# Kernel tuning notes

Measured on AMD Instinct MI355X. Metric: run time of the kernel, lower is better.

## Reference

```python
import jax, jax.numpy as jnp
import numpy as np

EMB = 128   # embedding_dim
ND = 128    # node_dim
B = 64      # graphs in batch
NN = 500    # n_nodes per graph
N = B * NN  # total nodes = 32000
E = 256000  # edges per edge set
M = 20      # history length in input_


def _lin_params(key, out_dim, in_dim, bias=True):
    k1, k2 = jax.random.split(key)
    s = 1.0 / np.sqrt(in_dim)
    w = jax.random.uniform(k1, (out_dim, in_dim), jnp.float32, -s, s)
    if bias:
        b = jax.random.uniform(k2, (out_dim,), jnp.float32, -s, s)
        return w, b
    return w


def setup_inputs() -> dict:
    key = jax.random.key(0)
    ks = jax.random.split(key, 40)
    inp = {}
    inp["state_"] = jax.random.normal(ks[0], (B, ND), jnp.float32)
    inp["input_"] = jax.random.normal(ks[1], (B, M, EMB), jnp.float32)
    inp["x"] = jax.random.normal(ks[2], (N, EMB), jnp.float32)
    inp["e_n"] = jax.random.randint(ks[3], (2, E), 0, N)
    inp["e_r0"] = jax.random.randint(ks[4], (2, E), 0, N)
    inp["e_r1"] = jax.random.randint(ks[5], (2, E), 0, N)
    inp["n_nodes"] = NN
    # GRU-like params
    inp["win"] = _lin_params(ks[6], ND, EMB, bias=False)
    inp["wz"], inp["bz"] = _lin_params(ks[7], ND, 2 * ND)
    inp["wr"], inp["br"] = _lin_params(ks[8], ND, 2 * ND)
    inp["wh"], inp["bh"] = _lin_params(ks[9], ND, 2 * ND)
    # GAT params: lin (out,in)+bias, attn (out, 2*out)+bias
    inp["g0_lw"], inp["g0_lb"] = _lin_params(ks[10], ND, EMB)
    inp["g0_aw"], inp["g0_ab"] = _lin_params(ks[11], ND, 2 * ND)
    inp["g1_lw"], inp["g1_lb"] = _lin_params(ks[12], ND, ND)
    inp["g1_aw"], inp["g1_ab"] = _lin_params(ks[13], ND, 2 * ND)
    inp["g2_lw"], inp["g2_lb"] = _lin_params(ks[14], ND, ND)
    inp["g2_aw"], inp["g2_ab"] = _lin_params(ks[15], ND, 2 * ND)
    inp["gn_lw"], inp["gn_lb"] = _lin_params(ks[16], ND, ND)
    inp["gn_aw"], inp["gn_ab"] = _lin_params(ks[17], ND, 2 * ND)
    # heads
    inp["pw"], inp["pb"] = _lin_params(ks[18], 1, ND)
    inp["mw"], inp["mb"] = _lin_params(ks[19], 1, ND)
    inp["sw"], inp["sb"] = _lin_params(ks[20], 1, ND)
    return inp


def gat_conv(x, ei, lw, lb, aw, ab, slope=0.2):
    """PyG GATConv variant: lin -> per-edge attn(cat(x_i,x_j)) -> leaky_relu ->
    per-dst segment softmax (per channel) -> scatter-add of x_j*alpha."""
    n = x.shape[0]
    sl = jnp.arange(n)
    src = jnp.concatenate([ei[0], sl])   # j (source)
    dst = jnp.concatenate([ei[1], sl])   # i (target; softmax + aggregation index)
    h = x @ lw.T + lb                    # [N, ND]
    hi = h[dst]                          # x_i  [E', ND]
    hj = h[src]                          # x_j  [E', ND]
    a = jnp.concatenate([hi, hj], axis=-1) @ aw.T + ab
    a = jax.nn.leaky_relu(a, slope)
    amax = jax.ops.segment_max(a, dst, num_segments=n)
    e = jnp.exp(a - amax[dst])
    denom = jax.ops.segment_sum(e, dst, num_segments=n)
    alpha = e / (denom[dst] + 1e-16)
    return jax.ops.segment_sum(hj * alpha, dst, num_segments=n)


def reference(state_, input_, x, e_n, e_r0, e_r1, n_nodes,
              win, wz, bz, wr, br, wh, bh,
              g0_lw, g0_lb, g0_aw, g0_ab,
              g1_lw, g1_lb, g1_aw, g1_ab,
              g2_lw, g2_lb, g2_aw, g2_ab,
              gn_lw, gn_lb, gn_aw, gn_ab,
              pw, pb, mw, mb, sw, sb):
    # GRU-like gated state update
    st = state_.reshape(-1, ND)
    inp = input_.reshape(st.shape[0], -1, EMB)
    i = jnp.mean(inp @ win.T, axis=1)              # [B, ND]
    si = jnp.concatenate([st, i], axis=-1)
    z = jax.nn.sigmoid(si @ wz.T + bz)
    r = jax.nn.sigmoid(si @ wr.T + br)
    hc = jnp.tanh(jnp.concatenate([r * st, i], axis=-1) @ wh.T + bh)
    h = (1 - z) * st + z * hc                      # [B, ND]

    # Stacked GAT layers
    g0 = gat_conv(x, e_n, g0_lw, g0_lb, g0_aw, g0_ab)
    g1 = gat_conv(g0, e_r1, g1_lw, g1_lb, g1_aw, g1_ab)
    g2 = gat_conv(g1, e_r1, g1_lw, g1_lb, g1_aw, g1_ab)
    g3 = gat_conv(g2, e_n, gn_lw, gn_lb, gn_aw, gn_ab) + g0
    g4 = gat_conv(g3, e_r0, g2_lw, g2_lb, g2_aw, g2_ab)
    g5 = gat_conv(g4, e_r0, g2_lw, g2_lb, g2_aw, g2_ab)
    gx = gat_conv(g5, e_n, gn_lw, gn_lb, gn_aw, gn_ab) + g3

    xg = gx.reshape(-1, n_nodes, ND)               # [B, NN, ND]
    xt = xg[:, 1:]                                 # skip depot node
    scores = (xt @ pw.T + pb)[..., 0]              # [B, NN-1]
    probs = jax.nn.softmax(scores, axis=-1)        # Categorical params
    a = jax.nn.elu((xt @ mw.T + mb)[..., 0]) + 2   # Beta alpha
    b = jax.nn.elu(jnp.abs((xt @ sw.T + sb)[..., 0])) + 2  # Beta beta
    return (h, probs, a, b)
```

## Files before the change

### kernel.cpp

```cpp
#include <hip/hip_runtime.h>
#include <hip/hip_bf16.h>

#define ND 128
#define EMB 128
#define BATCH 64
#define MM 20
#define NN 500
#define RPAD 8

typedef short bf16x8 __attribute__((ext_vector_type(8)));
typedef float f32x4 __attribute__((ext_vector_type(4)));

__device__ __forceinline__ float bf2f(unsigned short u) {
    union { unsigned int i; float f; } x; x.i = ((unsigned int)u) << 16; return x.f;
}
__device__ __forceinline__ unsigned short f2bf(float f) {
    union { float f; unsigned int i; } x; x.f = f;
    unsigned int r = x.i + 0x7fffu + ((x.i >> 16) & 1u);
    return (unsigned short)(r >> 16);
}
__device__ __forceinline__ float2 bfpair(unsigned int p) {
    union { unsigned int i; float f; } a, b;
    a.i = p << 16; b.i = p & 0xffff0000u;
    return make_float2(a.f, b.f);
}

struct EdgePtrs { const int* e[3]; };

__global__ void edge_hist3(EdgePtrs ep, int* __restrict__ cnt, int E, int N) {
    int li = blockIdx.y;
    const int* dst = ep.e[li] + E;
    int e = blockIdx.x * blockDim.x + threadIdx.x;
    if (e < E) atomicAdd(&cnt[(size_t)li * N + dst[e]], 1);
}

__global__ void exscan3(const int* __restrict__ cnt, int* __restrict__ rowptr, int n) {
    __shared__ int wsum[16];
    __shared__ int woff[16];
    int li = blockIdx.x;
    const int4* c4 = (const int4*)(cnt + (size_t)li * n);
    int* rp = rowptr + (size_t)li * (n + RPAD);
    int t = threadIdx.x;
    int lane = t & 63, wid = t >> 6;
    int n4 = n >> 2;

    int4 v[8];
    int s = 0;
#pragma unroll
    for (int i = 0; i < 8; ++i) {
        int idx = t * 8 + i;
        if (idx < n4) v[i] = c4[idx];
        else { v[i].x = v[i].y = v[i].z = v[i].w = 0; }
    }
#pragma unroll
    for (int i = 0; i < 8; ++i) s += v[i].x + v[i].y + v[i].z + v[i].w;

    int ps = s;
#pragma unroll
    for (int d = 1; d < 64; d <<= 1) {
        int u = __shfl_up(ps, d, 64);
        if (lane >= d) ps += u;
    }
    if (lane == 63) wsum[wid] = ps;
    __syncthreads();
    if (t == 0) {
        int r = 0;
        for (int i = 0; i < 16; ++i) { woff[i] = r; r += wsum[i]; }
    }
    __syncthreads();
    int run = woff[wid] + ps - s;
    int4* rp4 = (int4*)rp;
#pragma unroll
    for (int i = 0; i < 8; ++i) {
        int idx = t * 8 + i;
        if (idx < n4) {
            int4 o;
            o.x = run; run += v[i].x;
            o.y = run; run += v[i].y;
            o.z = run; run += v[i].z;
            o.w = run; run += v[i].w;
            rp4[idx] = o;
        }
    }
    if (t == (n - 1) / 32) rp[n] = run;
}

__global__ void edge_scatter3(EdgePtrs ep, const int* __restrict__ rowptr, int* __restrict__ cnt,
                              int* __restrict__ col, int E, int N) {
    int li = blockIdx.y;
    const int* src = ep.e[li];
    const int* dst = src + E;
    const int* rp = rowptr + (size_t)li * (N + RPAD);
    int e = blockIdx.x * blockDim.x + threadIdx.x;
    if (e < E) {
        int d = dst[e];
        int p = atomicSub(&cnt[(size_t)li * N + d], 1) - 1;
        col[(size_t)li * E + rp[d] + p] = src[e];
    }
}

struct WcPtrs {
    const float* lw[4]; const float* lb[4]; const float* aw[4]; const float* ab[4];
    unsigned short* Whi[4]; unsigned short* Wlo[4]; float* Bf[4];
};

__global__ void make_wc4(WcPtrs p) {
    int set = blockIdx.y;
    const float* lw = p.lw[set]; const float* lb = p.lb[set];
    const float* aw = p.aw[set]; const float* ab = p.ab[set];
    int n = blockIdx.x;
    int e = threadIdx.x;
    float w;
    if (n < 128) {
        w = lw[n * 128 + e];
    } else if (n < 256) {
        int ni = n - 128; float s = 0.f;
        for (int k = 0; k < 128; ++k) s += aw[ni * 256 + k] * lw[k * 128 + e];
        w = s;
    } else {
        int nj = n - 256; float s = 0.f;
        for (int k = 0; k < 128; ++k) s += aw[nj * 256 + 128 + k] * lw[k * 128 + e];
        w = s;
    }
    unsigned short hi = f2bf(w);
    p.Whi[set][n * 128 + e] = hi;
    p.Wlo[set][n * 128 + e] = f2bf(w - bf2f(hi));
    if (e == 0) {
        float b;
        if (n < 128) b = lb[n];
        else if (n < 256) {
            int ni = n - 128; float s = ab[ni];
            for (int k = 0; k < 128; ++k) s += aw[ni * 256 + k] * lb[k];
            b = s;
        } else {
            int nj = n - 256; float s = 0.f;
            for (int k = 0; k < 128; ++k) s += aw[nj * 256 + 128 + k] * lb[k];
            b = s;
        }
        p.Bf[set][n] = b;
    }
}

__launch_bounds__(384)
__global__ void lin_fused(const float* __restrict__ X,
                          const unsigned short* __restrict__ Whi,
                          const unsigned short* __restrict__ Wlo,
                          const float* __restrict__ bias,
                          void* __restrict__ hu, int M) {
    __shared__ __align__(16) unsigned short sxh[2][16][136];
    __shared__ __align__(16) unsigned short sxl[2][16][136];
    const int tid = threadIdx.x;
    const int slab = tid >> 6;
    const int lane = tid & 63;
    const int r16 = lane & 15;
    const int quad = lane >> 4;
    const int srow = tid >> 4;
    const int scol = (tid & 15) * 8;

    unsigned short* hu16 = (unsigned short*)hu;
    float* huf = (float*)hu;

    const unsigned short* Wh = Whi + (size_t)slab * 64 * 128;
    const unsigned short* Wl = Wlo + (size_t)slab * 64 * 128;
    bf16x8 wh[4][4], wl[4][4];
#pragma unroll
    for (int nt = 0; nt < 4; ++nt)
#pragma unroll
        for (int ks = 0; ks < 4; ++ks) {
            wh[nt][ks] = *(const bf16x8*)(Wh + (nt * 16 + r16) * 128 + ks * 32 + quad * 8);
            wl[nt][ks] = *(const bf16x8*)(Wl + (nt * 16 + r16) * 128 + ks * 32 + quad * 8);
        }
    float bv[4];
#pragma unroll
    for (int nt = 0; nt < 4; ++nt) bv[nt] = bias[slab * 64 + nt * 16 + r16];

    const int mt_count = M >> 4;
    const int G = gridDim.x;
    const int mt0 = blockIdx.x;

    {
        float v[8];
        if (tid < 256) {
            const float* xp = X + (size_t)(mt0 * 16 + srow) * 128 + scol;
            float4 v0 = *(const float4*)xp;
            float4 v1 = *(const float4*)(xp + 4);
            v[0] = v0.x; v[1] = v0.y; v[2] = v0.z; v[3] = v0.w;
            v[4] = v1.x; v[5] = v1.y; v[6] = v1.z; v[7] = v1.w;
            unsigned int hh[4], ll[4];
#pragma unroll
            for (int j = 0; j < 4; ++j) {
                unsigned short h0 = f2bf(v[2 * j]);
                unsigned short h1 = f2bf(v[2 * j + 1]);
                unsigned short l0 = f2bf(v[2 * j] - bf2f(h0));
                unsigned short l1 = f2bf(v[2 * j + 1] - bf2f(h1));
                hh[j] = (unsigned int)h0 | ((unsigned int)h1 << 16);
                ll[j] = (unsigned int)l0 | ((unsigned int)l1 << 16);
            }
            *(uint4*)&sxh[0][srow][scol] = make_uint4(hh[0], hh[1], hh[2], hh[3]);
            *(uint4*)&sxl[0][srow][scol] = make_uint4(ll[0], ll[1], ll[2], ll[3]);
        }
    }
    __syncthreads();

    int cur = 0;
    for (int mt = mt0; mt < mt_count; mt += G) {
        const int nxt = mt + G;
        const bool has = nxt < mt_count;

        float v[8];
        if (has && tid < 256) {
            const float* xp = X + (size_t)(nxt * 16 + srow) * 128 + scol;
            float4 v0 = *(const float4*)xp;
            float4 v1 = *(const float4*)(xp + 4);
            v[0] = v0.x; v[1] = v0.y; v[2] = v0.z; v[3] = v0.w;
            v[4] = v1.x; v[5] = v1.y; v[6] = v1.z; v[7] = v1.w;
        }

        bf16x8 ah[4], al[4];
#pragma unroll
        for (int ks = 0; ks < 4; ++ks) {
            ah[ks] = *(const bf16x8*)&sxh[cur][r16][ks * 32 + quad * 8];
            al[ks] = *(const bf16x8*)&sxl[cur][r16][ks * 32 + quad * 8];
        }

#pragma unroll
        for (int nt = 0; nt < 4; ++nt) {
            f32x4 acc = {bv[nt], bv[nt], bv[nt], bv[nt]};
#pragma unroll
            for (int ks = 0; ks < 4; ++ks) {
                acc = __builtin_amdgcn_mfma_f32_16x16x32_bf16(ah[ks], wh[nt][ks], acc, 0, 0, 0);
                acc = __builtin_amdgcn_mfma_f32_16x16x32_bf16(al[ks], wh[nt][ks], acc, 0, 0, 0);
                acc = __builtin_amdgcn_mfma_f32_16x16x32_bf16(ah[ks], wl[nt][ks], acc, 0, 0, 0);
            }
            int col = slab * 64 + nt * 16 + r16;
#pragma unroll
            for (int r = 0; r < 4; ++r) {
                size_t row = (size_t)(mt * 16 + quad * 4 + r);
                if (slab < 2) {
                    int c = col;
                    hu16[row * 512 + ((c & ~1) << 1) + (c & 1)] = f2bf(acc[r]);
                } else if (slab < 4) {
                    int c = col - 128;
                    huf[row * 256 + 128 + c] = acc[r];
                } else {
                    int c = col - 256;
                    hu16[row * 512 + ((c & ~1) << 1) + 2 + (c & 1)] = f2bf(acc[r]);
                }
            }
        }

        if (has && tid < 256) {
            unsigned int hh[4], ll[4];
#pragma unroll
            for (int j = 0; j < 4; ++j) {
                unsigned short h0 = f2bf(v[2 * j]);
                unsigned short h1 = f2bf(v[2 * j + 1]);
                unsigned short l0 = f2bf(v[2 * j] - bf2f(h0));
                unsigned short l1 = f2bf(v[2 * j + 1] - bf2f(h1));
                hh[j] = (unsigned int)h0 | ((unsigned int)h1 << 16);
                ll[j] = (unsigned int)l0 | ((unsigned int)l1 << 16);
            }
            *(uint4*)&sxh[cur ^ 1][srow][scol] = make_uint4(hh[0], hh[1], hh[2], hh[3]);
            *(uint4*)&sxl[cur ^ 1][srow][scol] = make_uint4(ll[0], ll[1], ll[2], ll[3]);
        }
        __syncthreads();
        cur ^= 1;
    }
}

__global__ void gat_agg(const void* __restrict__ hu,
                        const int* __restrict__ rowptr, const int* __restrict__ col,
                        const float* __restrict__ resid,
                        float* __restrict__ out, int N) {
    int wid = (int)((blockIdx.x * blockDim.x + threadIdx.x) >> 6);
    if (wid >= N) return;
    int lane = threadIdx.x & 63;
    const uint2* P = (const uint2*)hu;
    const float2* U = (const float2*)hu;

    float2 uiv = U[(size_t)wid * 128 + 64 + lane];
    uint2 sp = P[(size_t)wid * 128 + lane];
    float2 hs = bfpair(sp.x);
    float2 ujs = bfpair(sp.y);

    float a0 = uiv.x + ujs.x; a0 = a0 > 0.f ? a0 : 0.2f * a0;
    float a1 = uiv.y + ujs.y; a1 = a1 > 0.f ? a1 : 0.2f * a1;
    float m0 = a0, m1 = a1, l0 = 1.f, l1 = 1.f;
    float acc0 = hs.x, acc1 = hs.y;

#define AGG_STEP(pk)                                                      \
    {                                                                     \
        float2 hj = bfpair(pk.x);                                         \
        float2 uj = bfpair(pk.y);                                         \
        float b0 = uiv.x + uj.x; b0 = b0 > 0.f ? b0 : 0.2f * b0;          \
        float b1 = uiv.y + uj.y; b1 = b1 > 0.f ? b1 : 0.2f * b1;          \
        float n0 = fmaxf(m0, b0), n1 = fmaxf(m1, b1);                     \
        float s0 = __expf(m0 - n0), s1 = __expf(m1 - n1);                 \
        float p0 = __expf(b0 - n0), p1 = __expf(b1 - n1);                 \
        l0 = l0 * s0 + p0;            l1 = l1 * s1 + p1;                  \
        acc0 = acc0 * s0 + hj.x * p0; acc1 = acc1 * s1 + hj.y * p1;       \
        m0 = n0; m1 = n1;                                                 \
    }

    int e = rowptr[wid], end = rowptr[wid + 1];
    for (; e + 8 <= end; e += 8) {
        int s0i = col[e],     s1i = col[e + 1], s2i = col[e + 2], s3i = col[e + 3];
        int s4i = col[e + 4], s5i = col[e + 5], s6i = col[e + 6], s7i = col[e + 7];
        uint2 p0 = P[(size_t)s0i * 128 + lane];
        uint2 p1 = P[(size_t)s1i * 128 + lane];
        uint2 p2 = P[(size_t)s2i * 128 + lane];
        uint2 p3 = P[(size_t)s3i * 128 + lane];
        uint2 p4 = P[(size_t)s4i * 128 + lane];
        uint2 p5 = P[(size_t)s5i * 128 + lane];
        uint2 p6 = P[(size_t)s6i * 128 + lane];
        uint2 p7 = P[(size_t)s7i * 128 + lane];
        AGG_STEP(p0);
        AGG_STEP(p1);
        AGG_STEP(p2);
        AGG_STEP(p3);
        AGG_STEP(p4);
        AGG_STEP(p5);
        AGG_STEP(p6);
        AGG_STEP(p7);
    }
    for (; e + 4 <= end; e += 4) {
        int sA = col[e], sB = col[e + 1], sC = col[e + 2], sD = col[e + 3];
        uint2 pA = P[(size_t)sA * 128 + lane];
        uint2 pB = P[(size_t)sB * 128 + lane];
        uint2 pC = P[(size_t)sC * 128 + lane];
        uint2 pD = P[(size_t)sD * 128 + lane];
        AGG_STEP(pA);
        AGG_STEP(pB);
        AGG_STEP(pC);
        AGG_STEP(pD);
    }
    for (; e < end; ++e) {
        int sA = col[e];
        uint2 pA = P[(size_t)sA * 128 + lane];
        AGG_STEP(pA);
    }
#undef AGG_STEP

    float o0 = acc0 / (l0 + 1e-16f);
    float o1 = acc1 / (l1 + 1e-16f);
    if (resid) {
        float2 rv = ((const float2*)resid)[(size_t)wid * 64 + lane];
        o0 += rv.x; o1 += rv.y;
    }
    ((float2*)out)[(size_t)wid * 64 + lane] = make_float2(o0, o1);
}

__global__ void gru_kernel(const float* __restrict__ st_, const float* __restrict__ in_,
                           const float* __restrict__ win,
                           const float* __restrict__ wz, const float* __restrict__ bz,
                           const float* __restrict__ wr, const float* __restrict__ br,
                           const float* __restrict__ wh, const float* __restrict__ bh,
                           float* __restrict__ out) {
    __shared__ float sst[ND], sib[EMB], si[ND], srs[ND];
    int b = blockIdx.x, d = threadIdx.x;
    float s = 0.f;
    for (int m = 0; m < MM; ++m) s += in_[((size_t)b * MM + m) * EMB + d];
    sib[d] = s * (1.0f / MM);
    sst[d] = st_[b * ND + d];
    __syncthreads();
    float iv = 0.f;
    for (int e = 0; e < EMB; ++e) iv += sib[e] * win[d * EMB + e];
    si[d] = iv;
    __syncthreads();
    float za = bz[d], ra = br[d];
    for (int e = 0; e < ND; ++e) {
        za += sst[e] * wz[d * 2 * ND + e] + si[e] * wz[d * 2 * ND + ND + e];
        ra += sst[e] * wr[d * 2 * ND + e] + si[e] * wr[d * 2 * ND + ND + e];
    }
    float z = 1.f / (1.f + __expf(-za));
    float r = 1.f / (1.f + __expf(-ra));
    srs[d] = r * sst[d];
    __syncthreads();
    float ha = bh[d];
    for (int e = 0; e < ND; ++e)
        ha += srs[e] * wh[d * 2 * ND + e] + si[e] * wh[d * 2 * ND + ND + e];
    float hc = tanhf(ha);
    out[b * ND + d] = (1.f - z) * sst[d] + z * hc;
}

__global__ void heads_dots(const float* __restrict__ gx,
                           const float* __restrict__ pw_,
                           const float* __restrict__ mw_, const float* __restrict__ mb_,
                           const float* __restrict__ sw_, const float* __restrict__ sbias_,
                           float* __restrict__ scores, float* __restrict__ out) {
    int t = blockIdx.x;
    int lane = threadIdx.x & 63;
    int b = blockIdx.y * 4 + (threadIdx.x >> 6);
    const float2* g2 = (const float2*)gx;
    float2 pwv = ((const float2*)pw_)[lane];
    float2 mwv = ((const float2*)mw_)[lane];
    float2 swv = ((const float2*)sw_)[lane];
    int node = b * NN + 1 + t;
    float2 xv = g2[(size_t)node * 64 + lane];
    float dp = xv.x * pwv.x + xv.y * pwv.y;
    float dm = xv.x * mwv.x + xv.y * mwv.y;
    float ds = xv.x * swv.x + xv.y * swv.y;
    for (int off = 32; off; off >>= 1) {
        dp += __shfl_xor(dp, off);
        dm += __shfl_xor(dm, off);
        ds += __shfl_xor(ds, off);
    }
    if (lane == 0) {
        scores[(size_t)b * (NN - 1) + t] = dp;
        float av = dm + mb_[0]; av = av > 0.f ? av : (__expf(av) - 1.f);
        float bv = fabsf(ds + sbias_[0]);
        float* oA = out + BATCH * ND + (size_t)BATCH * (NN - 1);
        float* oB = oA + (size_t)BATCH * (NN - 1);
        oA[(size_t)b * (NN - 1) + t] = av + 2.f;
        oB[(size_t)b * (NN - 1) + t] = bv + 2.f;
    }
}

__global__ void heads_softmax(const float* __restrict__ scores, float* __restrict__ out) {
    __shared__ float scs[NN - 1], red[256];
    int b = blockIdx.x, tid = threadIdx.x;
    float mx = -1e30f;
    for (int t = tid; t < NN - 1; t += 256) { float v = scores[(size_t)b * (NN - 1) + t]; scs[t] = v; mx = fmaxf(mx, v); }
    red[tid] = mx; __syncthreads();
    for (int off = 128; off; off >>= 1) { if (tid < off) red[tid] = fmaxf(red[tid], red[tid + off]); __syncthreads(); }
    mx = red[0]; __syncthreads();
    float sum = 0.f;
    for (int t = tid; t < NN - 1; t += 256) { float e = __expf(scs[t] - mx); scs[t] = e; sum += e; }
    red[tid] = sum; __syncthreads();
    for (int off = 128; off; off >>= 1) { if (tid < off) red[tid] += red[tid + off]; __syncthreads(); }
    float inv = 1.0f / red[0];
    float* oP = out + BATCH * ND + (size_t)b * (NN - 1);
    for (int t = tid; t < NN - 1; t += 256) oP[t] = scs[t] * inv;
}

extern "C" void kernel_launch(void* const* d_in, const int* in_sizes, int n_in,
                              void* d_out, int out_size, void* d_ws, size_t ws_size,
                              hipStream_t stream) {
    const float* state_ = (const float*)d_in[0];
    const float* input_ = (const float*)d_in[1];
    const float* x      = (const float*)d_in[2];
    const int* e_n  = (const int*)d_in[3];
    const int* e_r0 = (const int*)d_in[4];
    const int* e_r1 = (const int*)d_in[5];
    const float* win = (const float*)d_in[7];
    const float* wz  = (const float*)d_in[8];
    const float* bz  = (const float*)d_in[9];
    const float* wr  = (const float*)d_in[10];
    const float* br  = (const float*)d_in[11];
    const float* wh  = (const float*)d_in[12];
    const float* bh  = (const float*)d_in[13];
    const float* pw = (const float*)d_in[30];
    const float* mw = (const float*)d_in[32];
    const float* mb = (const float*)d_in[33];
    const float* sw = (const float*)d_in[34];
    const float* sb = (const float*)d_in[35];
    float* out = (float*)d_out;

    const int E = in_sizes[3] / 2;
    const int N = in_sizes[2] / EMB;

    char* w = (char*)d_ws;
    auto alloc = [&](size_t bytes) { char* p = w; w += (bytes + 255) & ~(size_t)255; return p; };
    int* rpbase = (int*)alloc(3 * (size_t)(N + RPAD) * sizeof(int));
    int* colbase = (int*)alloc(3 * (size_t)E * sizeof(int));
    int* tmp = (int*)alloc(3 * (size_t)N * sizeof(int));
    unsigned short* Whi[4]; unsigned short* Wlo[4]; float* Bf[4];
    for (int i = 0; i < 4; ++i) {
        Whi[i] = (unsigned short*)alloc(384 * 128 * 2);
        Wlo[i] = (unsigned short*)alloc(384 * 128 * 2);
        Bf[i]  = (float*)alloc(384 * 4);
    }
    void* hu = (void*)alloc((size_t)N * 1024);
    float* ga = (float*)alloc((size_t)N * 128 * 4);
    float* gb = (float*)alloc((size_t)N * 128 * 4);
    float* gc = (float*)alloc((size_t)N * 128 * 4);
    float* scores = (float*)alloc((size_t)BATCH * (NN - 1) * 4);

    EdgePtrs ep; ep.e[0] = e_n; ep.e[1] = e_r0; ep.e[2] = e_r1;

    hipMemsetAsync(tmp, 0, 3 * (size_t)N * sizeof(int), stream);
    edge_hist3<<<dim3((E + 255) / 256, 3), 256, 0, stream>>>(ep, tmp, E, N);
    exscan3<<<3, 1024, 0, stream>>>(tmp, rpbase, N);
    edge_scatter3<<<dim3((E + 255) / 256, 3), 256, 0, stream>>>(ep, rpbase, tmp, colbase, E, N);

    WcPtrs wp;
    wp.lw[0] = (const float*)d_in[14]; wp.lb[0] = (const float*)d_in[15];
    wp.aw[0] = (const float*)d_in[16]; wp.ab[0] = (const float*)d_in[17];
    wp.lw[1] = (const float*)d_in[18]; wp.lb[1] = (const float*)d_in[19];
    wp.aw[1] = (const float*)d_in[20]; wp.ab[1] = (const float*)d_in[21];
    wp.lw[2] = (const float*)d_in[22]; wp.lb[2] = (const float*)d_in[23];
    wp.aw[2] = (const float*)d_in[24]; wp.ab[2] = (const float*)d_in[25];
    wp.lw[3] = (const float*)d_in[26]; wp.lb[3] = (const float*)d_in[27];
    wp.aw[3] = (const float*)d_in[28]; wp.ab[3] = (const float*)d_in[29];
    for (int i = 0; i < 4; ++i) { wp.Whi[i] = Whi[i]; wp.Wlo[i] = Wlo[i]; wp.Bf[i] = Bf[i]; }
    make_wc4<<<dim3(384, 4), 128, 0, stream>>>(wp);

    gru_kernel<<<BATCH, ND, 0, stream>>>(state_, input_, win, wz, bz, wr, br, wh, bh, out);

    auto conv = [&](const float* in, int csr_i, int wi, const float* resid, float* o) {
        lin_fused<<<512, 384, 0, stream>>>(in, Whi[wi], Wlo[wi], Bf[wi], hu, N);
        gat_agg<<<(N * 64) / 256, 256, 0, stream>>>(hu, rpbase + (size_t)csr_i * (N + RPAD),
                                                    colbase + (size_t)csr_i * E, resid, o, N);
    };

    conv(x,  0, 0, nullptr, ga);
    conv(ga, 2, 1, nullptr, gb);
    conv(gb, 2, 1, nullptr, gc);
    conv(gc, 0, 3, ga,      gb);
    conv(gb, 1, 2, nullptr, gc);
    conv(gc, 1, 2, nullptr, ga);
    conv(ga, 0, 3, gb,      gc);

    heads_dots<<<dim3(NN - 1, 16), 256, 0, stream>>>(gc, pw, mw, mb, sw, sb, scores, out);
    heads_softmax<<<BATCH, 256, 0, stream>>>(scores, out);
}
```

Baseline: 639.0 us.

## Fuse next layer's linear projection into GAT aggregation kernel epilogue

Each aggregation kernel now also computes the following layer's linear+attention projection for its 16 nodes using split-bf16 MFMA, writing the packed hu buffer for the next layer into a ping-pong buffer. This removes six separate lin_fused launches and the re-read of the fp32 layer output. In exchange it uses 1024-thread blocks with a block-wide sync after the irregular gather, so the slowest node in each group of 16 delays the whole block, and every block re-reads the weight matrix from global memory. It also needs N to be a multiple of 16, since the bounds check was removed.

New measurement: 862.1 us. 34.9% more time.

```diff
diff --git a/kernel.cpp b/kernel.cpp
--- a/kernel.cpp
+++ b/kernel.cpp
@@ -268,18 +268,28 @@
     }
 }
 
-__global__ void gat_agg(const void* __restrict__ hu,
-                        const int* __restrict__ rowptr, const int* __restrict__ col,
-                        const float* __restrict__ resid,
-                        float* __restrict__ out, int N) {
-    int wid = (int)((blockIdx.x * blockDim.x + threadIdx.x) >> 6);
-    if (wid >= N) return;
-    int lane = threadIdx.x & 63;
-    const uint2* P = (const uint2*)hu;
-    const float2* U = (const float2*)hu;
-
-    float2 uiv = U[(size_t)wid * 128 + 64 + lane];
-    uint2 sp = P[(size_t)wid * 128 + lane];
+__launch_bounds__(1024)
+__global__ void gat_agg_fused(const void* __restrict__ huIn,
+                              const int* __restrict__ rowptr, const int* __restrict__ col,
+                              const float* __restrict__ resid,
+                              float* __restrict__ out, int N,
+                              const unsigned short* __restrict__ Whi,
+                              const unsigned short* __restrict__ Wlo,
+                              const float* __restrict__ Bf,
+                              void* __restrict__ huOut) {
+    __shared__ __align__(16) unsigned short sxh[16][136];
+    __shared__ __align__(16) unsigned short sxl[16][136];
+    __shared__ __align__(16) unsigned short opk[16][520];
+    const int tid = threadIdx.x;
+    const int wave = tid >> 6;
+    const int lane = tid & 63;
+    const int node = blockIdx.x * 16 + wave;
+
+    const uint2* P = (const uint2*)huIn;
+    const float2* U = (const float2*)huIn;
+
+    float2 uiv = U[(size_t)node * 128 + 64 + lane];
+    uint2 sp = P[(size_t)node * 128 + lane];
     float2 hs = bfpair(sp.x);
     float2 ujs = bfpair(sp.y);
 
@@ -288,10 +298,10 @@
     float m0 = a0, m1 = a1, l0 = 1.f, l1 = 1.f;
     float acc0 = hs.x, acc1 = hs.y;
 
-#define AGG_STEP(pk)                                                      \
+#define AGG_STEP(pkv)                                                     \
     {                                                                     \
-        float2 hj = bfpair(pk.x);                                         \
-        float2 uj = bfpair(pk.y);                                         \
+        float2 hj = bfpair(pkv.x);                                        \
+        float2 uj = bfpair(pkv.y);                                        \
         float b0 = uiv.x + uj.x; b0 = b0 > 0.f ? b0 : 0.2f * b0;          \
         float b1 = uiv.y + uj.y; b1 = b1 > 0.f ? b1 : 0.2f * b1;          \
         float n0 = fmaxf(m0, b0), n1 = fmaxf(m1, b1);                     \
@@ -302,52 +312,100 @@
         m0 = n0; m1 = n1;                                                 \
     }
 
-    int e = rowptr[wid], end = rowptr[wid + 1];
+    int e = rowptr[node], end = rowptr[node + 1];
     for (; e + 8 <= end; e += 8) {
         int s0i = col[e],     s1i = col[e + 1], s2i = col[e + 2], s3i = col[e + 3];
         int s4i = col[e + 4], s5i = col[e + 5], s6i = col[e + 6], s7i = col[e + 7];
-        uint2 p0 = P[(size_t)s0i * 128 + lane];
-        uint2 p1 = P[(size_t)s1i * 128 + lane];
-        uint2 p2 = P[(size_t)s2i * 128 + lane];
-        uint2 p3 = P[(size_t)s3i * 128 + lane];
-        uint2 p4 = P[(size_t)s4i * 128 + lane];
-        uint2 p5 = P[(size_t)s5i * 128 + lane];
-        uint2 p6 = P[(size_t)s6i * 128 + lane];
-        uint2 p7 = P[(size_t)s7i * 128 + lane];
-        AGG_STEP(p0);
-        AGG_STEP(p1);
-        AGG_STEP(p2);
-        AGG_STEP(p3);
-        AGG_STEP(p4);
-        AGG_STEP(p5);
-        AGG_STEP(p6);
-        AGG_STEP(p7);
+        uint2 q0 = P[(size_t)s0i * 128 + lane];
+        uint2 q1 = P[(size_t)s1i * 128 + lane];
+        uint2 q2 = P[(size_t)s2i * 128 + lane];
+        uint2 q3 = P[(size_t)s3i * 128 + lane];
+        uint2 q4 = P[(size_t)s4i * 128 + lane];
+        uint2 q5 = P[(size_t)s5i * 128 + lane];
+        uint2 q6 = P[(size_t)s6i * 128 + lane];
+        uint2 q7 = P[(size_t)s7i * 128 + lane];
+        AGG_STEP(q0); AGG_STEP(q1); AGG_STEP(q2); AGG_STEP(q3);
+        AGG_STEP(q4); AGG_STEP(q5); AGG_STEP(q6); AGG_STEP(q7);
     }
     for (; e + 4 <= end; e += 4) {
         int sA = col[e], sB = col[e + 1], sC = col[e + 2], sD = col[e + 3];
-        uint2 pA = P[(size_t)sA * 128 + lane];
-        uint2 pB = P[(size_t)sB * 128 + lane];
-        uint2 pC = P[(size_t)sC * 128 + lane];
-        uint2 pD = P[(size_t)sD * 128 + lane];
-        AGG_STEP(pA);
-        AGG_STEP(pB);
-        AGG_STEP(pC);
-        AGG_STEP(pD);
+        uint2 qA = P[(size_t)sA * 128 + lane];
+        uint2 qB = P[(size_t)sB * 128 + lane];
+        uint2 qC = P[(size_t)sC * 128 + lane];
+        uint2 qD = P[(size_t)sD * 128 + lane];
+        AGG_STEP(qA); AGG_STEP(qB); AGG_STEP(qC); AGG_STEP(qD);
     }
     for (; e < end; ++e) {
         int sA = col[e];
-        uint2 pA = P[(size_t)sA * 128 + lane];
-        AGG_STEP(pA);
+        uint2 qA = P[(size_t)sA * 128 + lane];
+        AGG_STEP(qA);
     }
 #undef AGG_STEP
 
     float o0 = acc0 / (l0 + 1e-16f);
     float o1 = acc1 / (l1 + 1e-16f);
     if (resid) {
-        float2 rv = ((const float2*)resid)[(size_t)wid * 64 + lane];
+        float2 rv = ((const float2*)resid)[(size_t)node * 64 + lane];
         o0 += rv.x; o1 += rv.y;
     }
-    ((float2*)out)[(size_t)wid * 64 + lane] = make_float2(o0, o1);
+    ((float2*)out)[(size_t)node * 64 + lane] = make_float2(o0, o1);
+
+    if (!Whi) return;
+
+    {
+        unsigned short h0 = f2bf(o0), h1 = f2bf(o1);
+        unsigned short g0 = f2bf(o0 - bf2f(h0)), g1 = f2bf(o1 - bf2f(h1));
+        *(unsigned int*)&sxh[wave][2 * lane] = (unsigned int)h0 | ((unsigned int)h1 << 16);
+        *(unsigned int*)&sxl[wave][2 * lane] = (unsigned int)g0 | ((unsigned int)g1 << 16);
+    }
+    __syncthreads();
+
+    const int r16 = lane & 15;
+    const int quad = lane >> 4;
+    bf16x8 ah[4], al[4];
+#pragma unroll
+    for (int ks = 0; ks < 4; ++ks) {
+        ah[ks] = *(const bf16x8*)&sxh[r16][ks * 32 + quad * 8];
+        al[ks] = *(const bf16x8*)&sxl[r16][ks * 32 + quad * 8];
+    }
+
+    for (int t = wave; t < 24; t += 16) {
+        bf16x8 wh[4], wl[4];
+#pragma unroll
+        for (int ks = 0; ks < 4; ++ks) {
+            wh[ks] = *(const bf16x8*)(Whi + (size_t)(t * 16 + r16) * 128 + ks * 32 + quad * 8);
+            wl[ks] = *(const bf16x8*)(Wlo + (size_t)(t * 16 + r16) * 128 + ks * 32 + quad * 8);
+        }
+        float bv = Bf[t * 16 + r16];
+        f32x4 acc = {bv, bv, bv, bv};
+#pragma unroll
+        for (int ks = 0; ks < 4; ++ks) {
+            acc = __builtin_amdgcn_mfma_f32_16x16x32_bf16(ah[ks], wh[ks], acc, 0, 0, 0);
+            acc = __builtin_amdgcn_mfma_f32_16x16x32_bf16(al[ks], wh[ks], acc, 0, 0, 0);
+            acc = __builtin_amdgcn_mfma_f32_16x16x32_bf16(ah[ks], wl[ks], acc, 0, 0, 0);
+        }
+        int cc = t * 16 + r16;
+#pragma unroll
+        for (int r = 0; r < 4; ++r) {
+            int lrow = quad * 4 + r;
+            if (cc < 128) {
+                opk[lrow][((cc & ~1) << 1) + (cc & 1)] = f2bf(acc[r]);
+            } else if (cc < 256) {
+                int c = cc - 128;
+                *(float*)&opk[lrow][256 + 2 * c] = acc[r];
+            } else {
+                int c = cc - 256;
+                opk[lrow][((c & ~1) << 1) + 2 + (c & 1)] = f2bf(acc[r]);
+            }
+        }
+    }
+    __syncthreads();
+
+    {
+        int r = tid >> 6, l = tid & 63;
+        uint4 vv = *(const uint4*)&opk[r][l * 8];
+        *(uint4*)((char*)huOut + (size_t)(blockIdx.x * 16 + r) * 1024 + l * 16) = vv;
+    }
 }
 
 __global__ void gru_kernel(const float* __restrict__ st_, const float* __restrict__ in_,
@@ -470,7 +528,8 @@
         Wlo[i] = (unsigned short*)alloc(384 * 128 * 2);
         Bf[i]  = (float*)alloc(384 * 4);
     }
-    void* hu = (void*)alloc((size_t)N * 1024);
+    void* huA = (void*)alloc((size_t)N * 1024);
+    void* huB = (void*)alloc((size_t)N * 1024);
     float* ga = (float*)alloc((size_t)N * 128 * 4);
     float* gb = (float*)alloc((size_t)N * 128 * 4);
     float* gc = (float*)alloc((size_t)N * 128 * 4);
@@ -497,19 +556,23 @@
 
     gru_kernel<<<BATCH, ND, 0, stream>>>(state_, input_, win, wz, bz, wr, br, wh, bh, out);
 
-    auto conv = [&](const float* in, int csr_i, int wi, const float* resid, float* o) {
-        lin_fused<<<512, 384, 0, stream>>>(in, Whi[wi], Wlo[wi], Bf[wi], hu, N);
-        gat_agg<<<(N * 64) / 256, 256, 0, stream>>>(hu, rpbase + (size_t)csr_i * (N + RPAD),
-                                                    colbase + (size_t)csr_i * E, resid, o, N);
-    };
-
-    conv(x,  0, 0, nullptr, ga);
-    conv(ga, 2, 1, nullptr, gb);
-    conv(gb, 2, 1, nullptr, gc);
-    conv(gc, 0, 3, ga,      gb);
-    conv(gb, 1, 2, nullptr, gc);
-    conv(gc, 1, 2, nullptr, ga);
-    conv(ga, 0, 3, gb,      gc);
+    lin_fused<<<512, 384, 0, stream>>>(x, Whi[0], Wlo[0], Bf[0], huA, N);
+
+    const int* rp0 = rpbase;
+    const int* rp1 = rpbase + (size_t)1 * (N + RPAD);
+    const int* rp2 = rpbase + (size_t)2 * (N + RPAD);
+    const int* cl0 = colbase;
+    const int* cl1 = colbase + (size_t)1 * E;
+    const int* cl2 = colbase + (size_t)2 * E;
+    const int GB = N / 16;
+
+    gat_agg_fused<<<GB, 1024, 0, stream>>>(huA, rp0, cl0, nullptr, ga, N, Whi[1], Wlo[1], Bf[1], huB);
+    gat_agg_fused<<<GB, 1024, 0, stream>>>(huB, rp2, cl2, nullptr, gb, N, Whi[1], Wlo[1], Bf[1], huA);
+    gat_agg_fused<<<GB, 1024, 0, stream>>>(huA, rp2, cl2, nullptr, gc, N, Whi[3], Wlo[3], Bf[3], huB);
+    gat_agg_fused<<<GB, 1024, 0, stream>>>(huB, rp0, cl0, ga,      gb, N, Whi[2], Wlo[2], Bf[2], huA);
+    gat_agg_fused<<<GB, 1024, 0, stream>>>(huA, rp1, cl1, nullptr, gc, N, Whi[2], Wlo[2], Bf[2], huB);
+    gat_agg_fused<<<GB, 1024, 0, stream>>>(huB, rp1, cl1, nullptr, ga, N, Whi[3], Wlo[3], Bf[3], huA);
+    gat_agg_fused<<<GB, 1024, 0, stream>>>(huA, rp0, cl0, gb,      gc, N, nullptr, nullptr, nullptr, nullptr);
 
     heads_dots<<<dim3(NN - 1, 16), 256, 0, stream>>>(gc, pw, mw, mb, sw, sb, scores, out);
     heads_softmax<<<BATCH, 256, 0, stream>>>(scores, out);
```
